# Kernel tuning notes

Hardware: AMD Instinct MI355X
Metric: run time of the kernel (lower is better)

The kernel has to match this reference:

```python
import jax, jax.numpy as jnp
import numpy as np

HID = 2880
NQ = 64
NKV = 8
HD = 64
THETA = 150000.0
WINDOW = 128
S = 8192


def _rope(x, positions):
    # x: [S, H, D]; half-split (rotate_half) convention
    d = x.shape[-1]
    inv_freq = 1.0 / (THETA ** (jnp.arange(0, d, 2, dtype=jnp.float32) / d))  # [D/2]
    ang = positions.astype(jnp.float32)[:, None] * inv_freq[None, :]          # [S, D/2]
    cos = jnp.cos(ang)[:, None, :]
    sin = jnp.sin(ang)[:, None, :]
    x1, x2 = jnp.split(x, 2, axis=-1)
    return jnp.concatenate([x1 * cos - x2 * sin, x2 * cos + x1 * sin], axis=-1)


def setup_inputs() -> dict:
    key = jax.random.key(0)
    ks = jax.random.split(key, 12)
    sd = 0.02
    return {
        "hidden": jax.random.normal(ks[0], (S, HID), dtype=jnp.float32),
        "positions": jnp.arange(S, dtype=jnp.int64) if jax.config.jax_enable_x64 else jnp.arange(S, dtype=jnp.int32),
        "Wq": jax.random.normal(ks[1], (HID, NQ * HD), dtype=jnp.float32) * sd,
        "bq": jax.random.normal(ks[2], (NQ * HD,), dtype=jnp.float32) * sd,
        "Wk": jax.random.normal(ks[3], (HID, NKV * HD), dtype=jnp.float32) * sd,
        "bk": jax.random.normal(ks[4], (NKV * HD,), dtype=jnp.float32) * sd,
        "Wv": jax.random.normal(ks[5], (HID, NKV * HD), dtype=jnp.float32) * sd,
        "bv": jax.random.normal(ks[6], (NKV * HD,), dtype=jnp.float32) * sd,
        "Wo": jax.random.normal(ks[7], (NQ * HD, HID), dtype=jnp.float32) * sd,
        "bo": jax.random.normal(ks[8], (HID,), dtype=jnp.float32) * sd,
    }


def _attention(hidden, positions, Wq, bq, Wk, bk, Wv, bv, Wo, bo):
    n_tok = hidden.shape[0]
    q = (hidden @ Wq + bq).reshape(n_tok, NQ, HD)
    k = (hidden @ Wk + bk).reshape(n_tok, NKV, HD)
    v = (hidden @ Wv + bv).reshape(n_tok, NKV, HD)
    q = _rope(q, positions)
    k = _rope(k, positions)

    # Blocked sliding-window causal attention (window == block size W).
    W = WINDOW
    nb = n_tok // W
    group = NQ // NKV
    qb = q.reshape(nb, W, NQ, HD)
    kb = k.reshape(nb, W, NKV, HD)
    vb = v.reshape(nb, W, NKV, HD)
    # each query block attends to its own block plus the previous one (2W keys)
    k_prev = jnp.concatenate([jnp.zeros_like(kb[:1]), kb[:-1]], axis=0)
    v_prev = jnp.concatenate([jnp.zeros_like(vb[:1]), vb[:-1]], axis=0)
    k_ctx = jnp.concatenate([k_prev, kb], axis=1)   # [nb, 2W, NKV, HD]
    v_ctx = jnp.concatenate([v_prev, vb], axis=1)
    # GQA: repeat KV heads to match query heads
    k_ctx = jnp.repeat(k_ctx, group, axis=2)        # [nb, 2W, NQ, HD]
    v_ctx = jnp.repeat(v_ctx, group, axis=2)

    scale = 1.0 / np.sqrt(HD)
    scores = jnp.einsum('bqhd,bkhd->bhqk', qb, k_ctx) * scale  # [nb, NQ, W, 2W]

    qi = jnp.arange(W)[:, None]            # local query pos
    ki = jnp.arange(2 * W)[None, :]        # local key pos within context
    diff = qi - ki + W                     # i - j (global)
    band = (diff >= 0) & (diff < WINDOW)   # causal + window
    kpos = jnp.arange(nb)[:, None, None] * W + ki[None] - W  # global key pos
    mask = band[None] & (kpos >= 0)        # [nb, W, 2W]

    neg = jnp.finfo(scores.dtype).min
    scores = jnp.where(mask[:, None, :, :], scores, neg)
    p = jax.nn.softmax(scores, axis=-1)
    attn = jnp.einsum('bhqk,bkhd->bqhd', p, v_ctx)  # [nb, W, NQ, HD]
    attn = attn.reshape(n_tok, NQ * HD)
    return attn @ Wo + bo


def reference(hidden, positions, Wq, bq, Wk, bk, Wv, bv, Wo, bo):
    return _attention(hidden, positions, Wq, bq, Wk, bk, Wv, bv, Wo, bo)
```

## Files before the change

### kernel.cpp

```cpp
#include <hip/hip_runtime.h>
#include <stdint.h>

#define S_TOK 8192
#define HID 2880
#define NQ 64
#define NKV 8
#define HD 64
#define QKV_N 5120
#define NO_PAD 2944

typedef __attribute__((ext_vector_type(8))) __bf16 bf16x8;
typedef __attribute__((ext_vector_type(4))) float f32x4;
typedef __attribute__((ext_vector_type(16))) float f32x16;

__device__ __forceinline__ unsigned short f2bf(float f) {
  unsigned int u = __builtin_bit_cast(unsigned int, f);
  u += 0x7fff + ((u >> 16) & 1);
  return (unsigned short)(u >> 16);
}
__device__ __forceinline__ float bf2f(unsigned short h) {
  unsigned int u = ((unsigned int)h) << 16;
  return __builtin_bit_cast(float, u);
}

__device__ __forceinline__ void async_lds16(const void* g, void* l) {
  __builtin_amdgcn_global_load_lds(
      (const __attribute__((address_space(1))) unsigned int*)g,
      (__attribute__((address_space(3))) unsigned int*)l, 16, 0, 0);
}

__global__ __launch_bounds__(256) void cvt_bf16_kernel(
    const float* __restrict__ src, unsigned short* __restrict__ dst) {
  size_t i = ((size_t)blockIdx.x * 256 + threadIdx.x) * 8;
  float4 a = *(const float4*)(src + i);
  float4 b = *(const float4*)(src + i + 4);
  union { unsigned short u[8]; uint4 v; } o;
  o.u[0] = f2bf(a.x); o.u[1] = f2bf(a.y); o.u[2] = f2bf(a.z); o.u[3] = f2bf(a.w);
  o.u[4] = f2bf(b.x); o.u[5] = f2bf(b.y); o.u[6] = f2bf(b.z); o.u[7] = f2bf(b.w);
  *(uint4*)(dst + i) = o.v;
}

__global__ __launch_bounds__(256) void transpose_cvt(
    const float* __restrict__ src, unsigned short* __restrict__ dst,
    int R, int C, int rowOff) {
  __shared__ float tile[32][33];
  int tx = threadIdx.x, ty = threadIdx.y;
  int c0 = blockIdx.x * 32, r0 = blockIdx.y * 32;
#pragma unroll
  for (int i = 0; i < 4; ++i)
    tile[ty + i * 8][tx] = src[(size_t)(r0 + ty + i * 8) * C + c0 + tx];
  __syncthreads();
#pragma unroll
  for (int i = 0; i < 4; ++i)
    dst[(size_t)(c0 + ty + i * 8 + rowOff) * R + r0 + tx] = f2bf(tile[tx][ty + i * 8]);
}

__global__ __launch_bounds__(256) void rope_kernel(
    unsigned short* __restrict__ qkv, const int* __restrict__ positions) {
  int gid = blockIdx.x * 256 + threadIdx.x;
  int d = gid & 31;
  int rest = gid >> 5;
  int head = rest % 72;
  int t = rest / 72;
  unsigned short* p = qkv + (size_t)t * QKV_N + head * 64;
  float x1 = bf2f(p[d]);
  float x2 = bf2f(p[d + 32]);
  float pos = (float)positions[t];
  float inv = exp2f(-0.5373313430f * (float)d);
  float ang = pos * inv;
  float s = sinf(ang), c = cosf(ang);
  p[d] = f2bf(x1 * c - x2 * s);
  p[d + 32] = f2bf(x2 * c + x1 * s);
}

template <int MODE>
__global__ __launch_bounds__(256) void gemm_bt(
    const unsigned short* __restrict__ A, const unsigned short* __restrict__ BT,
    void* __restrict__ Cout, int K,
    const float* __restrict__ b0, const float* __restrict__ b1,
    const float* __restrict__ b2) {
  __shared__ unsigned short lds[128 * 128];
  unsigned short* As = lds;
  unsigned short* Bs = lds + 128 * 64;
  const int tid = threadIdx.x;
  const int wave = tid >> 6, lane = tid & 63;
  const int l31 = lane & 31, lh = lane >> 5;
  const int wy = wave >> 1, wx = wave & 1;
  const int m0 = blockIdx.y * 128, n0 = blockIdx.x * 128;

  f32x16 acc[2][2];
#pragma unroll
  for (int i = 0; i < 2; ++i)
#pragma unroll
    for (int j = 0; j < 2; ++j)
#pragma unroll
      for (int r = 0; r < 16; ++r) acc[i][j][r] = 0.f;

  for (int k0 = 0; k0 < K; k0 += 64) {
    const unsigned short* Ag = A + (size_t)m0 * K + k0;
    const unsigned short* Bg = BT + (size_t)n0 * K + k0;
#pragma unroll
    for (int i = 0; i < 4; ++i) {
      int s = tid + i * 256;
      int row = s >> 3;
      int c = (s & 7) ^ (row & 7);
      async_lds16(Ag + (size_t)row * K + c * 8, &As[s * 8]);
      async_lds16(Bg + (size_t)row * K + c * 8, &Bs[s * 8]);
    }
    __syncthreads();
#pragma unroll
    for (int ks = 0; ks < 4; ++ks) {
      bf16x8 af[2], bfr[2];
#pragma unroll
      for (int ra = 0; ra < 2; ++ra) {
        int row = wy * 64 + ra * 32 + l31;
        int p = (ks * 2 + lh) ^ (row & 7);
        af[ra] = *(const bf16x8*)&As[row * 64 + p * 8];
      }
#pragma unroll
      for (int cb = 0; cb < 2; ++cb) {
        int row = wx * 64 + cb * 32 + l31;
        int p = (ks * 2 + lh) ^ (row & 7);
        bfr[cb] = *(const bf16x8*)&Bs[row * 64 + p * 8];
      }
#pragma unroll
      for (int ra = 0; ra < 2; ++ra)
#pragma unroll
        for (int cb = 0; cb < 2; ++cb)
          acc[ra][cb] = __builtin_amdgcn_mfma_f32_32x32x16_bf16(
              af[ra], bfr[cb], acc[ra][cb], 0, 0, 0);
    }
    __syncthreads();
  }

  if (MODE == 0) {
#pragma unroll
    for (int cb = 0; cb < 2; ++cb) {
      int col = wx * 64 + cb * 32 + l31;
      int gcol = n0 + col;
      float bias = (gcol < 4096) ? b0[gcol]
                                 : (gcol < 4608 ? b1[gcol - 4096] : b2[gcol - 4608]);
#pragma unroll
      for (int ra = 0; ra < 2; ++ra) {
#pragma unroll
        for (int r = 0; r < 16; ++r) {
          int row = wy * 64 + ra * 32 + (r & 3) + 8 * (r >> 2) + 4 * lh;
          lds[row * 128 + col] = f2bf(acc[ra][cb][r] + bias);
        }
      }
    }
    __syncthreads();
    unsigned short* C16 = (unsigned short*)Cout;
#pragma unroll
    for (int i = 0; i < 8; ++i) {
      int s = tid + i * 256;
      int row = s >> 4, cc = (s & 15) * 8;
      *(uint4*)(C16 + (size_t)(m0 + row) * QKV_N + n0 + cc) =
          *(const uint4*)&lds[row * 128 + cc];
    }
  } else {
#pragma unroll
    for (int cb = 0; cb < 2; ++cb) {
      int gcol = n0 + wx * 64 + cb * 32 + l31;
      if (gcol < HID) {
        float bias = b0[gcol];
#pragma unroll
        for (int ra = 0; ra < 2; ++ra) {
#pragma unroll
          for (int r = 0; r < 16; ++r) {
            int row = m0 + wy * 64 + ra * 32 + (r & 3) + 8 * (r >> 2) + 4 * lh;
            ((float*)Cout)[(size_t)row * HID + gcol] = acc[ra][cb][r] + bias;
          }
        }
      }
    }
  }
}

__global__ __launch_bounds__(256) void attn_kernel(
    const unsigned short* __restrict__ qkv, unsigned short* __restrict__ attn) {
  __shared__ unsigned short Qs[64 * 72];
  __shared__ unsigned short Ks[192 * 72];
  __shared__ unsigned short VTs[64 * 200];

  const int tid = threadIdx.x;
  const int B = blockIdx.x;
  const int h = blockIdx.y;
  const int hk = h >> 3;
  const int wave = tid >> 6, lane = tid & 63;
  const int quad = lane >> 4, ml = lane & 15;

#pragma unroll
  for (int it = 0; it < 2; ++it) {
    int s = tid + it * 256;
    int row = s >> 3, c = (s & 7) << 3;
    *(uint4*)&Qs[row * 72 + c] =
        *(const uint4*)(qkv + (size_t)(B * 64 + row) * QKV_N + h * 64 + c);
  }
#pragma unroll
  for (int it = 0; it < 6; ++it) {
    int s = tid + it * 256;
    int j = s >> 3, c = (s & 7) << 3;
    int tk = B * 64 - 128 + j;
    uint4 kv = make_uint4(0, 0, 0, 0), vv = make_uint4(0, 0, 0, 0);
    if (tk >= 0) {
      kv = *(const uint4*)(qkv + (size_t)tk * QKV_N + 4096 + hk * 64 + c);
      vv = *(const uint4*)(qkv + (size_t)tk * QKV_N + 4608 + hk * 64 + c);
    }
    *(uint4*)&Ks[j * 72 + c] = kv;
    union { uint4 q; unsigned short u[8]; } vu;
    vu.q = vv;
#pragma unroll
    for (int e = 0; e < 8; ++e) VTs[(c + e) * 200 + j] = vu.u[e];
  }
  __syncthreads();

  f32x4 zero = {0.f, 0.f, 0.f, 0.f};
  f32x4 sc[12];
#pragma unroll
  for (int jn = 0; jn < 12; ++jn) sc[jn] = zero;
#pragma unroll
  for (int kk = 0; kk < 2; ++kk) {
    bf16x8 af = *(const bf16x8*)&Qs[(wave * 16 + ml) * 72 + kk * 32 + quad * 8];
#pragma unroll
    for (int jn = 0; jn < 12; ++jn) {
      bf16x8 bfr = *(const bf16x8*)&Ks[(jn * 16 + ml) * 72 + kk * 32 + quad * 8];
      sc[jn] = __builtin_amdgcn_mfma_f32_16x16x32_bf16(af, bfr, sc[jn], 0, 0, 0);
    }
  }

  const float NEG = -3.0e38f;
  float mx[4], sm[4];
#pragma unroll
  for (int r = 0; r < 4; ++r) mx[r] = NEG;
#pragma unroll
  for (int jn = 0; jn < 12; ++jn) {
    int j = jn * 16 + ml;
#pragma unroll
    for (int r = 0; r < 4; ++r) {
      int i = wave * 16 + quad * 4 + r;
      bool valid = (j > i) && (j <= i + 128) && (B * 64 + j - 128 >= 0);
      float v = valid ? sc[jn][r] * 0.125f : NEG;
      sc[jn][r] = v;
      mx[r] = fmaxf(mx[r], v);
    }
  }
#pragma unroll
  for (int r = 0; r < 4; ++r) {
#pragma unroll
    for (int off = 1; off < 16; off <<= 1)
      mx[r] = fmaxf(mx[r], __shfl_xor(mx[r], off, 64));
    sm[r] = 0.f;
  }
#pragma unroll
  for (int jn = 0; jn < 12; ++jn) {
#pragma unroll
    for (int r = 0; r < 4; ++r) {
      float p = expf(sc[jn][r] - mx[r]);
      sc[jn][r] = p;
      sm[r] += p;
    }
  }
#pragma unroll
  for (int r = 0; r < 4; ++r) {
#pragma unroll
    for (int off = 1; off < 16; off <<= 1) sm[r] += __shfl_xor(sm[r], off, 64);
    sm[r] = 1.0f / sm[r];
  }
  __syncthreads();

  unsigned short* P = Ks;
#pragma unroll
  for (int jn = 0; jn < 12; ++jn) {
#pragma unroll
    for (int r = 0; r < 4; ++r)
      P[(wave * 16 + quad * 4 + r) * 200 + jn * 16 + ml] = f2bf(sc[jn][r] * sm[r]);
  }
  __syncthreads();

  f32x4 ov[4];
#pragma unroll
  for (int jn = 0; jn < 4; ++jn) ov[jn] = zero;
#pragma unroll
  for (int ks = 0; ks < 6; ++ks) {
    bf16x8 af = *(const bf16x8*)&P[(wave * 16 + ml) * 200 + ks * 32 + quad * 8];
#pragma unroll
    for (int jn = 0; jn < 4; ++jn) {
      bf16x8 bfr = *(const bf16x8*)&VTs[(jn * 16 + ml) * 200 + ks * 32 + quad * 8];
      ov[jn] = __builtin_amdgcn_mfma_f32_16x16x32_bf16(af, bfr, ov[jn], 0, 0, 0);
    }
  }
#pragma unroll
  for (int jn = 0; jn < 4; ++jn) {
#pragma unroll
    for (int r = 0; r < 4; ++r) {
      int row = B * 64 + wave * 16 + quad * 4 + r;
      attn[(size_t)row * 4096 + h * 64 + jn * 16 + ml] = f2bf(ov[jn][r]);
    }
  }
}

extern "C" void kernel_launch(void* const* d_in, const int* in_sizes, int n_in,
                              void* d_out, int out_size, void* d_ws, size_t ws_size,
                              hipStream_t stream) {
  const float* hidden = (const float*)d_in[0];
  const int* positions = (const int*)d_in[1];
  const float* Wq = (const float*)d_in[2];
  const float* bq = (const float*)d_in[3];
  const float* Wk = (const float*)d_in[4];
  const float* bk = (const float*)d_in[5];
  const float* Wv = (const float*)d_in[6];
  const float* bv = (const float*)d_in[7];
  const float* Wo = (const float*)d_in[8];
  const float* bo = (const float*)d_in[9];
  float* out = (float*)d_out;

  char* ws = (char*)d_ws;
  unsigned short* A_h   = (unsigned short*)(ws);
  unsigned short* BTqkv = (unsigned short*)(ws + 47185920);
  unsigned short* qkv   = (unsigned short*)(ws + 76677120);
  unsigned short* BTo   = (unsigned short*)(ws + 160563200);
  unsigned short* attn  = (unsigned short*)(ws);

  cvt_bf16_kernel<<<11520, 256, 0, stream>>>(hidden, A_h);
  dim3 tb(32, 8);
  transpose_cvt<<<dim3(128, 90), tb, 0, stream>>>(Wq, BTqkv, HID, 4096, 0);
  transpose_cvt<<<dim3(16, 90), tb, 0, stream>>>(Wk, BTqkv, HID, 512, 4096);
  transpose_cvt<<<dim3(16, 90), tb, 0, stream>>>(Wv, BTqkv, HID, 512, 4608);
  transpose_cvt<<<dim3(90, 128), tb, 0, stream>>>(Wo, BTo, 4096, HID, 0);
  hipMemsetAsync(BTo + (size_t)HID * 4096, 0, (size_t)(NO_PAD - HID) * 4096 * 2, stream);

  gemm_bt<0><<<dim3(QKV_N / 128, S_TOK / 128), 256, 0, stream>>>(
      A_h, BTqkv, qkv, HID, bq, bk, bv);
  rope_kernel<<<73728, 256, 0, stream>>>(qkv, positions);
  attn_kernel<<<dim3(S_TOK / 64, NQ), 256, 0, stream>>>(qkv, attn);
  gemm_bt<1><<<dim3(NO_PAD / 128, S_TOK / 128), 256, 0, stream>>>(
      attn, BTo, out, 4096, bo, nullptr, nullptr);
}
```

Before: 977.7 us.

## Replace GEMM with 256x128 triple-buffered async-LDS pipelined kernel

Rewrites both projection GEMMs as a 512-thread kernel with 256x128 tiles and a three-stage LDS ring. Global-to-LDS loads for tile t+2 are issued in halves between the MFMA phases, with explicit waitcnt, barriers and setprio. The MFMA shape moves from 32x32x16 to 16x16x32. The goal is to hide global load latency and raise per-block reuse, at the cost of larger LDS use (144KB per block), hand-tuned vmcnt counts that must match the issue order, and fewer blocks in the grid.

After: 904.4 us. 7.5% less time.

```diff
diff --git a/kernel.cpp b/kernel.cpp
--- a/kernel.cpp
+++ b/kernel.cpp
@@ -11,7 +11,6 @@
 
 typedef __attribute__((ext_vector_type(8))) __bf16 bf16x8;
 typedef __attribute__((ext_vector_type(4))) float f32x4;
-typedef __attribute__((ext_vector_type(16))) float f32x16;
 
 __device__ __forceinline__ unsigned short f2bf(float f) {
   unsigned int u = __builtin_bit_cast(unsigned int, f);
@@ -27,6 +26,12 @@
   __builtin_amdgcn_global_load_lds(
       (const __attribute__((address_space(1))) unsigned int*)g,
       (__attribute__((address_space(3))) unsigned int*)l, 16, 0, 0);
+}
+
+__device__ __forceinline__ void wg_barrier() {
+  asm volatile("" ::: "memory");
+  __builtin_amdgcn_s_barrier();
+  asm volatile("" ::: "memory");
 }
 
 __global__ __launch_bounds__(256) void cvt_bf16_kernel(
@@ -74,104 +79,166 @@
 }
 
 template <int MODE>
-__global__ __launch_bounds__(256) void gemm_bt(
+__global__ __launch_bounds__(512, 2) void gemm256(
     const unsigned short* __restrict__ A, const unsigned short* __restrict__ BT,
-    void* __restrict__ Cout, int K,
+    void* __restrict__ Cout, int K, int NT,
     const float* __restrict__ b0, const float* __restrict__ b1,
     const float* __restrict__ b2) {
-  __shared__ unsigned short lds[128 * 128];
-  unsigned short* As = lds;
-  unsigned short* Bs = lds + 128 * 64;
+  __shared__ unsigned short lds[3 * 24576];
   const int tid = threadIdx.x;
-  const int wave = tid >> 6, lane = tid & 63;
-  const int l31 = lane & 31, lh = lane >> 5;
-  const int wy = wave >> 1, wx = wave & 1;
-  const int m0 = blockIdx.y * 128, n0 = blockIdx.x * 128;
-
-  f32x16 acc[2][2];
-#pragma unroll
-  for (int i = 0; i < 2; ++i)
-#pragma unroll
-    for (int j = 0; j < 2; ++j)
-#pragma unroll
-      for (int r = 0; r < 16; ++r) acc[i][j][r] = 0.f;
-
-  for (int k0 = 0; k0 < K; k0 += 64) {
-    const unsigned short* Ag = A + (size_t)m0 * K + k0;
-    const unsigned short* Bg = BT + (size_t)n0 * K + k0;
-#pragma unroll
-    for (int i = 0; i < 4; ++i) {
-      int s = tid + i * 256;
+  const int lane = tid & 63;
+  const int wid = tid >> 6;
+  const int wy = wid >> 2, wx = wid & 3;
+  const int l15 = lane & 15, l4 = lane >> 4;
+  const int m0 = blockIdx.y * 256, n0 = blockIdx.x * 128;
+
+  const unsigned short* Ag = A + (size_t)m0 * K;
+  const unsigned short* Bg = BT + (size_t)n0 * K;
+
+  f32x4 acc[8][2];
+#pragma unroll
+  for (int m = 0; m < 8; ++m)
+#pragma unroll
+    for (int n = 0; n < 2; ++n)
+#pragma unroll
+      for (int r = 0; r < 4; ++r) acc[m][n][r] = 0.f;
+
+  auto stageA = [&](int t, int buf) {
+    unsigned short* dst = lds + buf * 24576;
+    const unsigned short* G = Ag + t * 64;
+#pragma unroll
+    for (int rd = 0; rd < 4; ++rd) {
+      int s = tid + rd * 512;
       int row = s >> 3;
-      int c = (s & 7) ^ (row & 7);
-      async_lds16(Ag + (size_t)row * K + c * 8, &As[s * 8]);
-      async_lds16(Bg + (size_t)row * K + c * 8, &Bs[s * 8]);
-    }
-    __syncthreads();
-#pragma unroll
-    for (int ks = 0; ks < 4; ++ks) {
-      bf16x8 af[2], bfr[2];
-#pragma unroll
-      for (int ra = 0; ra < 2; ++ra) {
-        int row = wy * 64 + ra * 32 + l31;
-        int p = (ks * 2 + lh) ^ (row & 7);
-        af[ra] = *(const bf16x8*)&As[row * 64 + p * 8];
+      int g = (s & 7) ^ (row & 7);
+      async_lds16(G + (size_t)row * K + g * 8, &dst[s * 8]);
+    }
+  };
+  auto stageB = [&](int t, int buf) {
+    unsigned short* dst = lds + buf * 24576 + 16384;
+    const unsigned short* G = Bg + t * 64;
+#pragma unroll
+    for (int rd = 0; rd < 2; ++rd) {
+      int s = tid + rd * 512;
+      int row = s >> 3;
+      int g = (s & 7) ^ (row & 7);
+      async_lds16(G + (size_t)row * K + g * 8, &dst[s * 8]);
+    }
+  };
+
+  stageA(0, 0); stageB(0, 0);
+  stageA(1, 1); stageB(1, 1);
+  asm volatile("s_waitcnt vmcnt(6)" ::: "memory");
+  wg_barrier();
+
+  int cur = 0, nxt = 2;
+  for (int t = 0; t < NT; ++t) {
+    const unsigned short* As = lds + cur * 24576;
+    const unsigned short* Bs = As + 16384;
+    bf16x8 bfrag[2][2], af0[4][2], af1[4][2];
+
+#pragma unroll
+    for (int n = 0; n < 2; ++n)
+#pragma unroll
+      for (int ks = 0; ks < 2; ++ks) {
+        int row = wx * 32 + n * 16 + l15;
+        int ch = (ks * 4 + l4) ^ (row & 7);
+        bfrag[n][ks] = *(const bf16x8*)&Bs[row * 64 + ch * 8];
       }
 #pragma unroll
-      for (int cb = 0; cb < 2; ++cb) {
-        int row = wx * 64 + cb * 32 + l31;
-        int p = (ks * 2 + lh) ^ (row & 7);
-        bfr[cb] = *(const bf16x8*)&Bs[row * 64 + p * 8];
+    for (int m = 0; m < 4; ++m)
+#pragma unroll
+      for (int ks = 0; ks < 2; ++ks) {
+        int row = wy * 128 + m * 16 + l15;
+        int ch = (ks * 4 + l4) ^ (row & 7);
+        af0[m][ks] = *(const bf16x8*)&As[row * 64 + ch * 8];
       }
-#pragma unroll
-      for (int ra = 0; ra < 2; ++ra)
-#pragma unroll
-        for (int cb = 0; cb < 2; ++cb)
-          acc[ra][cb] = __builtin_amdgcn_mfma_f32_32x32x16_bf16(
-              af[ra], bfr[cb], acc[ra][cb], 0, 0, 0);
-    }
-    __syncthreads();
-  }
+    if (t + 2 < NT) stageA(t + 2, nxt);
+    wg_barrier();
+    asm volatile("s_waitcnt lgkmcnt(0)" ::: "memory");
+    __builtin_amdgcn_sched_barrier(0);
+    __builtin_amdgcn_s_setprio(1);
+#pragma unroll
+    for (int m = 0; m < 4; ++m)
+#pragma unroll
+      for (int n = 0; n < 2; ++n)
+#pragma unroll
+        for (int ks = 0; ks < 2; ++ks)
+          acc[m][n] = __builtin_amdgcn_mfma_f32_16x16x32_bf16(
+              af0[m][ks], bfrag[n][ks], acc[m][n], 0, 0, 0);
+    __builtin_amdgcn_s_setprio(0);
+    wg_barrier();
+
+#pragma unroll
+    for (int m = 0; m < 4; ++m)
+#pragma unroll
+      for (int ks = 0; ks < 2; ++ks) {
+        int row = wy * 128 + (m + 4) * 16 + l15;
+        int ch = (ks * 4 + l4) ^ (row & 7);
+        af1[m][ks] = *(const bf16x8*)&As[row * 64 + ch * 8];
+      }
+    if (t + 2 < NT) stageB(t + 2, nxt);
+    wg_barrier();
+    asm volatile("s_waitcnt lgkmcnt(0)" ::: "memory");
+    __builtin_amdgcn_sched_barrier(0);
+    __builtin_amdgcn_s_setprio(1);
+#pragma unroll
+    for (int m = 0; m < 4; ++m)
+#pragma unroll
+      for (int n = 0; n < 2; ++n)
+#pragma unroll
+        for (int ks = 0; ks < 2; ++ks)
+          acc[m + 4][n] = __builtin_amdgcn_mfma_f32_16x16x32_bf16(
+              af1[m][ks], bfrag[n][ks], acc[m + 4][n], 0, 0, 0);
+    __builtin_amdgcn_s_setprio(0);
+    if (t + 2 < NT) { asm volatile("s_waitcnt vmcnt(6)" ::: "memory"); }
+    else            { asm volatile("s_waitcnt vmcnt(0)" ::: "memory"); }
+    wg_barrier();
+    cur = (cur == 2) ? 0 : cur + 1;
+    nxt = (nxt == 2) ? 0 : nxt + 1;
+  }
+  __syncthreads();
 
   if (MODE == 0) {
-#pragma unroll
-    for (int cb = 0; cb < 2; ++cb) {
-      int col = wx * 64 + cb * 32 + l31;
+    unsigned short* ldsC = lds;
+#pragma unroll
+    for (int n = 0; n < 2; ++n) {
+      int col = wx * 32 + n * 16 + l15;
       int gcol = n0 + col;
       float bias = (gcol < 4096) ? b0[gcol]
                                  : (gcol < 4608 ? b1[gcol - 4096] : b2[gcol - 4608]);
 #pragma unroll
-      for (int ra = 0; ra < 2; ++ra) {
-#pragma unroll
-        for (int r = 0; r < 16; ++r) {
-          int row = wy * 64 + ra * 32 + (r & 3) + 8 * (r >> 2) + 4 * lh;
-          lds[row * 128 + col] = f2bf(acc[ra][cb][r] + bias);
+      for (int m = 0; m < 8; ++m)
+#pragma unroll
+        for (int r = 0; r < 4; ++r) {
+          int row = wy * 128 + m * 16 + l4 * 4 + r;
+          ldsC[row * 136 + col] = f2bf(acc[m][n][r] + bias);
         }
-      }
     }
     __syncthreads();
     unsigned short* C16 = (unsigned short*)Cout;
 #pragma unroll
     for (int i = 0; i < 8; ++i) {
-      int s = tid + i * 256;
-      int row = s >> 4, cc = (s & 15) * 8;
+      int s = tid + i * 512;
+      int row = s >> 4;
+      int cc = (s & 15) * 8;
       *(uint4*)(C16 + (size_t)(m0 + row) * QKV_N + n0 + cc) =
-          *(const uint4*)&lds[row * 128 + cc];
+          *(const uint4*)&ldsC[row * 136 + cc];
     }
   } else {
-#pragma unroll
-    for (int cb = 0; cb < 2; ++cb) {
-      int gcol = n0 + wx * 64 + cb * 32 + l31;
+    float* Cf = (float*)Cout;
+#pragma unroll
+    for (int n = 0; n < 2; ++n) {
+      int gcol = n0 + wx * 32 + n * 16 + l15;
       if (gcol < HID) {
         float bias = b0[gcol];
 #pragma unroll
-        for (int ra = 0; ra < 2; ++ra) {
-#pragma unroll
-          for (int r = 0; r < 16; ++r) {
-            int row = m0 + wy * 64 + ra * 32 + (r & 3) + 8 * (r >> 2) + 4 * lh;
-            ((float*)Cout)[(size_t)row * HID + gcol] = acc[ra][cb][r] + bias;
+        for (int m = 0; m < 8; ++m)
+#pragma unroll
+          for (int r = 0; r < 4; ++r) {
+            int row = m0 + wy * 128 + m * 16 + l4 * 4 + r;
+            Cf[(size_t)row * HID + gcol] = acc[m][n][r] + bias;
           }
-        }
       }
     }
   }
@@ -330,10 +397,10 @@
   transpose_cvt<<<dim3(90, 128), tb, 0, stream>>>(Wo, BTo, 4096, HID, 0);
   hipMemsetAsync(BTo + (size_t)HID * 4096, 0, (size_t)(NO_PAD - HID) * 4096 * 2, stream);
 
-  gemm_bt<0><<<dim3(QKV_N / 128, S_TOK / 128), 256, 0, stream>>>(
-      A_h, BTqkv, qkv, HID, bq, bk, bv);
+  gemm256<0><<<dim3(QKV_N / 128, S_TOK / 256), 512, 0, stream>>>(
+      A_h, BTqkv, qkv, HID, HID / 64, bq, bk, bv);
   rope_kernel<<<73728, 256, 0, stream>>>(qkv, positions);
   attn_kernel<<<dim3(S_TOK / 64, NQ), 256, 0, stream>>>(qkv, attn);
-  gemm_bt<1><<<dim3(NO_PAD / 128, S_TOK / 128), 256, 0, stream>>>(
-      attn, BTo, out, 4096, bo, nullptr, nullptr);
-}
+  gemm256<1><<<dim3(NO_PAD / 128, S_TOK / 256), 512, 0, stream>>>(
+      attn, BTo, out, 4096, 4096 / 64, bo, nullptr, nullptr);
+}
```
